# Kernel optimization log

Hardware: AMD Instinct MI355X
Metric: run time of the kernel (lower is better)

Reference implementation:

```python
import jax, jax.numpy as jnp
import numpy as np
import math

N_AGENTS = 512
TRAJ_LEN = 16
TAU = 2048          # obs_shape + n_actions = 1536 + 512
MSG = 32768         # messages_shape
HID = 512           # args.hidden_dim
DV = MSG // N_AGENTS  # 64, per-agent message dim


def setup_inputs() -> dict:
    key = jax.random.key(0)
    ks = jax.random.split(key, 8)
    s = 0.02
    return {
        "imagined_trajectory": jax.random.normal(ks[0], (TRAJ_LEN, N_AGENTS, TAU), jnp.float32),
        "received_messages": jax.random.normal(ks[1], (N_AGENTS, MSG), jnp.float32),
        "Wq": jax.random.normal(ks[2], (MSG, HID), jnp.float32) * s,
        "bq": jnp.zeros((HID,), jnp.float32),
        "Wk": jax.random.normal(ks[3], (TAU, HID), jnp.float32) * s,
        "bk": jnp.zeros((HID,), jnp.float32),
        "Wv": jax.random.normal(ks[4], (TAU, DV), jnp.float32) * s,
        "bv": jnp.zeros((DV,), jnp.float32),
    }


def reference(imagined_trajectory, received_messages, Wq, bq, Wk, bk, Wv, bv):
    # q: [N, H]
    q = received_messages @ Wq + bq
    T, N, tau = imagined_trajectory.shape
    taus = imagined_trajectory.reshape(T * N, tau)          # row j*N + i == (traj step j, agent i)
    k = (taus @ Wk + bk).reshape(T, N, HID)                 # [T, N, H]
    v = (taus @ Wv + bv).reshape(T, N, DV)                  # [T, N, Dv]
    # per-agent dot-product attention over trajectory steps (vectorized form of
    # the original double python loop: score[i, j] = dot(q[i], k[j*N+i]) / sqrt(H))
    scores = jnp.einsum("nh,tnh->nt", q, k) / math.sqrt(HID)  # [N, T]
    alpha = jax.nn.softmax(scores, axis=-1)
    messages = jnp.einsum("nt,tnd->nd", alpha, v)           # [N, Dv]
    return messages
```

## Files before the change

### kernel.cpp

```cpp
#include <hip/hip_runtime.h>
#include <hip/hip_fp16.h>

#define N_AG 512
#define TRAJ 16
#define TAU_ 2048
#define MSG_ 32768
#define HID_ 512
#define DV_ 64
#define NTOT 576
#define SPLITQ 32
#define LDS_K 40
#define BUFH (128 * LDS_K)

typedef _Float16 f16x8 __attribute__((ext_vector_type(8)));
typedef _Float16 f16x4 __attribute__((ext_vector_type(4)));
typedef _Float16 f16x2 __attribute__((ext_vector_type(2)));
typedef __fp16 h16x2 __attribute__((ext_vector_type(2)));
typedef float f32x4 __attribute__((ext_vector_type(4)));

#define VMCNT(n) asm volatile("s_waitcnt vmcnt(" #n ")" ::: "memory")
#define LGKM0    asm volatile("s_waitcnt lgkmcnt(0)" ::: "memory")
#define BAR()    __builtin_amdgcn_s_barrier()
#define SCHED0() __builtin_amdgcn_sched_barrier(0)

__device__ __forceinline__ void gload16(const void* g, void* l) {
    __builtin_amdgcn_global_load_lds(
        (const __attribute__((address_space(1))) void*)g,
        (__attribute__((address_space(3))) void*)l, 16, 0, 0);
}

__global__ __launch_bounds__(256) void prep(const float* __restrict__ Wk,
                                            const float* __restrict__ Wv,
                                            const float* __restrict__ bk,
                                            const float* __restrict__ bv,
                                            _Float16* __restrict__ Wt,
                                            float* __restrict__ bb)
{
    __shared__ float td[64][65];
    const int kt = blockIdx.x;
    const int nt = blockIdx.y;
    const int k0 = kt * 64;
    const bool isv = (nt == 8);
    const float* src = isv ? Wv : Wk;
    const int ldsrc = isv ? DV_ : HID_;
    const int ncol0 = isv ? 0 : nt * 64;
    for (int e = threadIdx.x; e < 4096; e += 256) {
        const int ki = e >> 6, ni = e & 63;
        td[ki][ni] = src[(size_t)(k0 + ki) * ldsrc + ncol0 + ni];
    }
    __syncthreads();
    for (int e = threadIdx.x; e < 4096; e += 256) {
        const int ni = e >> 6, ki = e & 63;
        Wt[(size_t)(nt * 64 + ni) * TAU_ + k0 + ki] = (_Float16)td[ki][ni];
    }
    if (kt == 0 && threadIdx.x < 64) {
        const int ng = nt * 64 + threadIdx.x;
        bb[ng] = isv ? bv[threadIdx.x] : bk[ng];
    }
}

__device__ __forceinline__ void gemm_tile128(
    _Float16* __restrict__ As, _Float16* __restrict__ Bs,
    const float* __restrict__ Ag, int lda,
    const float* __restrict__ Bg, int ldb,
    _Float16* __restrict__ Cg, int ldc, int K)
{
    const int tid = threadIdx.x;
    const int lane = tid & 63;
    const int wid = tid >> 6;
    const int wr = wid >> 1;
    const int wc = wid & 1;
    const int am = tid >> 1;
    const int ak = (tid & 1) << 4;
    const int btn = tid & 31;
    const int btk = tid >> 5;
    const int arow = wr * 64 + (lane & 15);
    const int brow = wc * 64 + (lane & 15);
    const int kblk = (lane >> 4) << 3;

    f32x4 acc[4][4];
#pragma unroll
    for (int mi = 0; mi < 4; ++mi)
#pragma unroll
        for (int ni = 0; ni < 4; ++ni)
            acc[mi][ni] = (f32x4){0.f, 0.f, 0.f, 0.f};

    float4 rA[8], rB[8];
    const int nt = K >> 5;

    auto load_stage = [&](float4 (&r)[8], int ks) {
        const float* ap = Ag + (size_t)am * lda + ks + ak;
#pragma unroll
        for (int i = 0; i < 4; ++i) r[i] = *(const float4*)(ap + 4 * i);
        const float* bp = Bg + (size_t)(ks + btk * 4) * ldb + btn * 4;
#pragma unroll
        for (int i = 0; i < 4; ++i) r[4 + i] = *(const float4*)(bp + (size_t)i * ldb);
    };
    auto write_stage = [&](float4 (&r)[8], int buf) {
        _Float16* abase = As + buf * BUFH + am * LDS_K + ak;
        const float* fa = (const float*)&r[0];
        f16x8 h0, h1;
#pragma unroll
        for (int i = 0; i < 8; ++i) { h0[i] = (_Float16)fa[i]; h1[i] = (_Float16)fa[8 + i]; }
        *(f16x8*)abase = h0;
        *(f16x8*)(abase + 8) = h1;
        const float* fb = (const float*)&r[4];
#pragma unroll
        for (int j = 0; j < 4; ++j) {
            f16x4 w;
#pragma unroll
            for (int i = 0; i < 4; ++i) w[i] = (_Float16)fb[i * 4 + j];
            *(f16x4*)(Bs + buf * BUFH + (btn * 4 + j) * LDS_K + btk * 4) = w;
        }
    };
    auto compute = [&](int buf) {
        const _Float16* ab = As + buf * BUFH;
        const _Float16* bbp = Bs + buf * BUFH;
        f16x8 af[4], bf[4];
#pragma unroll
        for (int mi = 0; mi < 4; ++mi)
            af[mi] = *(const f16x8*)(ab + (arow + mi * 16) * LDS_K + kblk);
#pragma unroll
        for (int ni = 0; ni < 4; ++ni)
            bf[ni] = *(const f16x8*)(bbp + (brow + ni * 16) * LDS_K + kblk);
#pragma unroll
        for (int mi = 0; mi < 4; ++mi)
#pragma unroll
            for (int ni = 0; ni < 4; ++ni)
                acc[mi][ni] = __builtin_amdgcn_mfma_f32_16x16x32_f16(
                    af[mi], bf[ni], acc[mi][ni], 0, 0, 0);
    };

    load_stage(rA, 0);
    load_stage(rB, 32);
    write_stage(rA, 0);
    __syncthreads();
    for (int t = 0; t < nt; t += 2) {
        if (t + 2 < nt) load_stage(rA, (t + 2) << 5);
        compute(0);
        if (t + 1 < nt) write_stage(rB, 1);
        __syncthreads();
        if (t + 3 < nt) load_stage(rB, (t + 3) << 5);
        compute(1);
        if (t + 2 < nt) write_stage(rA, 0);
        __syncthreads();
    }
#pragma unroll
    for (int mi = 0; mi < 4; ++mi)
#pragma unroll
        for (int ni = 0; ni < 4; ++ni) {
            const int row = wr * 64 + mi * 16 + ((lane >> 4) << 2);
            const int col = wc * 64 + ni * 16 + (lane & 15);
#pragma unroll
            for (int r = 0; r < 4; ++r)
                Cg[(size_t)(row + r) * ldc + col] = (_Float16)acc[mi][ni][r];
        }
}

__global__ __launch_bounds__(256, 2) void qgemm(const float* __restrict__ X,
                                                const float* __restrict__ Wq,
                                                _Float16* __restrict__ qpart)
{
    __shared__ __align__(16) _Float16 smem[4 * BUFH];
    const int b = blockIdx.x;
    const int w = (b & 7) * 64 + (b >> 3);
    const int s = w >> 4;
    const int bm = (w >> 2) & 3;
    const int bn = w & 3;
    const int KS = MSG_ / SPLITQ;
    gemm_tile128(smem, smem + 2 * BUFH,
                 X + (size_t)bm * 128 * MSG_ + s * KS, MSG_,
                 Wq + (size_t)(s * KS) * HID_ + bn * 128, HID_,
                 qpart + (size_t)s * (N_AG * HID_) + bm * 128 * HID_ + bn * 128, HID_,
                 KS);
}

__global__ __launch_bounds__(256, 2) void kvgemm(const float* __restrict__ A,
                                                 const _Float16* __restrict__ Wt,
                                                 const float* __restrict__ bb,
                                                 _Float16* __restrict__ cmat)
{
    __shared__ __align__(1024) char smem[32768];
    const int tid = threadIdx.x;
    const int l = tid & 63;
    const int w = tid >> 6;

    const int b = blockIdx.x;
    const int wsw = (b & 7) * 48 + (b >> 3);
    const int bm = wsw / 3;
    const int bn = wsw % 3;
    const int m0 = bm * 64;
    const int n0 = bn * 192;

    const int arow = tid >> 2;
    const int aslot = (tid & 3) ^ ((tid >> 3) & 3);
    const float* ag = A + (size_t)(m0 + arow) * TAU_ + (tid & 3) * 8;
    char* const alds = smem + arow * 64 + aslot * 16;

    const int bsrcc = (l & 3) ^ ((l >> 3) & 3);

    const int r15 = l & 15;
    const int swz = ((l >> 4) ^ ((r15 >> 1) & 3)) * 16;

    f32x4 acc[4][3];
#pragma unroll
    for (int mi = 0; mi < 4; ++mi)
#pragma unroll
        for (int ni = 0; ni < 3; ++ni)
            acc[mi][ni] = (f32x4){0.f, 0.f, 0.f, 0.f};

    float4 r0[2], r1[2];

    auto aload = [&](float4 (&r)[2], int t) {
        const float* p = ag + t * 32;
        r[0] = *(const float4*)(p);
        r[1] = *(const float4*)(p + 4);
    };
    auto awrite = [&](float4 (&r)[2], int parity) {
        union { h16x2 h2[4]; f16x8 v; } u;
        const float* f = (const float*)&r[0];
        u.h2[0] = __builtin_amdgcn_cvt_pkrtz(f[0], f[1]);
        u.h2[1] = __builtin_amdgcn_cvt_pkrtz(f[2], f[3]);
        u.h2[2] = __builtin_amdgcn_cvt_pkrtz(f[4], f[5]);
        u.h2[3] = __builtin_amdgcn_cvt_pkrtz(f[6], f[7]);
        *(f16x8*)(alds + parity * 4096) = u.v;
    };
    auto bdma = [&](int t, int parity) {
        char* base = smem + 8192 + parity * 12288;
#pragma unroll
        for (int jj = 0; jj < 3; ++jj) {
            const int j = w * 3 + jj;
            const int row = 16 * j + (l >> 2);
            const _Float16* gp = Wt + (size_t)(n0 + row) * TAU_ + t * 32 + bsrcc * 8;
            gload16(gp, base + j * 1024);
        }
    };
    auto compute = [&](int parity) {
        const char* ab = smem + parity * 4096;
        const char* bbp = smem + 8192 + parity * 12288;
        f16x8 af[4], bf[3];
#pragma unroll
        for (int mi = 0; mi < 4; ++mi)
            af[mi] = *(const f16x8*)(ab + (mi * 16 + r15) * 64 + swz);
#pragma unroll
        for (int ni = 0; ni < 3; ++ni)
            bf[ni] = *(const f16x8*)(bbp + (w * 48 + ni * 16 + r15) * 64 + swz);
        __builtin_amdgcn_s_setprio(1);
#pragma unroll
        for (int mi = 0; mi < 4; ++mi)
#pragma unroll
            for (int ni = 0; ni < 3; ++ni)
                acc[mi][ni] = __builtin_amdgcn_mfma_f32_16x16x32_f16(
                    af[mi], bf[ni], acc[mi][ni], 0, 0, 0);
        __builtin_amdgcn_s_setprio(0);
    };

    bdma(0, 0); aload(r0, 0);
    bdma(1, 1); aload(r1, 1);
    VMCNT(5);
    awrite(r0, 0);
    LGKM0;

    for (int t = 0; t < 62; t += 2) {
        BAR(); SCHED0();
        compute(0);
        SCHED0(); BAR();
        bdma(t + 2, 0); aload(r0, t + 2);
        VMCNT(5);
        awrite(r1, 1);
        LGKM0;

        BAR(); SCHED0();
        compute(1);
        SCHED0(); BAR();
        bdma(t + 3, 1); aload(r1, t + 3);
        VMCNT(5);
        awrite(r0, 0);
        LGKM0;
    }
    BAR(); SCHED0();
    compute(0);
    SCHED0(); BAR();
    VMCNT(0);
    awrite(r1, 1);
    LGKM0;
    BAR(); SCHED0();
    compute(1);

#pragma unroll
    for (int mi = 0; mi < 4; ++mi)
#pragma unroll
        for (int ni = 0; ni < 3; ++ni) {
            const int row = m0 + mi * 16 + ((l >> 4) << 2);
            const int col = n0 + w * 48 + ni * 16 + r15;
            const float badd = bb[col];
#pragma unroll
            for (int r = 0; r < 4; ++r)
                cmat[(size_t)(row + r) * NTOT + col] = (_Float16)(acc[mi][ni][r] + badd);
        }
}

__global__ __launch_bounds__(256) void attn(const _Float16* __restrict__ qpart,
                                            const _Float16* __restrict__ cmat,
                                            const float* __restrict__ bq,
                                            const float* __restrict__ bv,
                                            float* __restrict__ out)
{
    const int n = blockIdx.x;
    const int tid = threadIdx.x;
    __shared__ float qs[HID_];
    __shared__ float scr[TRAJ];

    {
        const int h2 = tid * 2;
        float a0 = bq[h2], a1 = bq[h2 + 1];
#pragma unroll
        for (int s = 0; s < SPLITQ; ++s) {
            f16x2 p = *(const f16x2*)(qpart + (size_t)s * (N_AG * HID_) + n * HID_ + h2);
            a0 += (float)p[0];
            a1 += (float)p[1];
        }
        qs[h2] = a0;
        qs[h2 + 1] = a1;
    }
    __syncthreads();

    const int w = tid >> 6;
    const int lane = tid & 63;
#pragma unroll
    for (int tt = 0; tt < 4; ++tt) {
        const int t = w * 4 + tt;
        const _Float16* kr = cmat + (size_t)(t * N_AG + n) * NTOT;
        const int h0 = lane * 8;
        f16x8 kv = *(const f16x8*)(kr + h0);
        float p = 0.f;
#pragma unroll
        for (int i = 0; i < 8; ++i) p += qs[h0 + i] * (float)kv[i];
#pragma unroll
        for (int off = 32; off > 0; off >>= 1) p += __shfl_xor(p, off);
        if (lane == 0) scr[t] = p;
    }
    __syncthreads();

    const float inv = 0.04419417382415922f;
    float sv[TRAJ];
    float mx = -1e30f;
#pragma unroll
    for (int t = 0; t < TRAJ; ++t) { sv[t] = scr[t] * inv; mx = fmaxf(mx, sv[t]); }
    float ssum = 0.f;
#pragma unroll
    for (int t = 0; t < TRAJ; ++t) { sv[t] = expf(sv[t] - mx); ssum += sv[t]; }
    const float rs = 1.f / ssum;

    if (tid < DV_) {
        float o = bv[tid];
#pragma unroll
        for (int t = 0; t < TRAJ; ++t)
            o += sv[t] * rs * (float)cmat[(size_t)(t * N_AG + n) * NTOT + HID_ + tid];
        out[n * DV_ + tid] = o;
    }
}

extern "C" void kernel_launch(void* const* d_in, const int* in_sizes, int n_in,
                              void* d_out, int out_size, void* d_ws, size_t ws_size,
                              hipStream_t stream)
{
    const float* traj = (const float*)d_in[0];
    const float* msgs = (const float*)d_in[1];
    const float* Wq   = (const float*)d_in[2];
    const float* bq   = (const float*)d_in[3];
    const float* Wk   = (const float*)d_in[4];
    const float* bk   = (const float*)d_in[5];
    const float* Wv   = (const float*)d_in[6];
    const float* bv   = (const float*)d_in[7];
    float* out = (float*)d_out;

    _Float16* qpart = (_Float16*)d_ws;
    _Float16* cmat  = qpart + (size_t)SPLITQ * N_AG * HID_;
    _Float16* Wt    = cmat + (size_t)TRAJ * N_AG * NTOT;
    float*    bb    = (float*)(Wt + (size_t)NTOT * TAU_);

    prep<<<dim3(32, 9), 256, 0, stream>>>(Wk, Wv, bk, bv, Wt, bb);
    qgemm<<<512, 256, 0, stream>>>(msgs, Wq, qpart);
    kvgemm<<<384, 256, 0, stream>>>(traj, Wt, bb, cmat);
    attn<<<512, 256, 0, stream>>>(qpart, cmat, bq, bv, out);
}
```

Before: 95.78 us.

## Deepen kvgemm pipeline from double to quad-buffered LDS stages

Changes the kv projection GEMM from a 2-stage to a 4-stage software pipeline. Three tiles of the fp32 A operand are held in registers and the B tiles are DMA'd into LDS ahead of compute, so more global-memory latency is hidden. LDS use doubles to 64KB per block, which may limit blocks per CU under the launch bounds of 2 and adds register pressure from the extra float4 staging sets.

```diff
diff --git a/kernel.cpp b/kernel.cpp
--- a/kernel.cpp
+++ b/kernel.cpp
@@ -180,7 +180,7 @@
                                                  const float* __restrict__ bb,
                                                  _Float16* __restrict__ cmat)
 {
-    __shared__ __align__(1024) char smem[32768];
+    __shared__ __align__(1024) char smem[65536];
     const int tid = threadIdx.x;
     const int l = tid & 63;
     const int w = tid >> 6;
@@ -209,24 +209,24 @@
         for (int ni = 0; ni < 3; ++ni)
             acc[mi][ni] = (f32x4){0.f, 0.f, 0.f, 0.f};
 
-    float4 r0[2], r1[2];
+    float4 r0[2], r1[2], r2[2], r3[2];
 
     auto aload = [&](float4 (&r)[2], int t) {
         const float* p = ag + t * 32;
         r[0] = *(const float4*)(p);
         r[1] = *(const float4*)(p + 4);
     };
-    auto awrite = [&](float4 (&r)[2], int parity) {
+    auto awrite = [&](float4 (&r)[2], int set) {
         union { h16x2 h2[4]; f16x8 v; } u;
         const float* f = (const float*)&r[0];
         u.h2[0] = __builtin_amdgcn_cvt_pkrtz(f[0], f[1]);
         u.h2[1] = __builtin_amdgcn_cvt_pkrtz(f[2], f[3]);
         u.h2[2] = __builtin_amdgcn_cvt_pkrtz(f[4], f[5]);
         u.h2[3] = __builtin_amdgcn_cvt_pkrtz(f[6], f[7]);
-        *(f16x8*)(alds + parity * 4096) = u.v;
-    };
-    auto bdma = [&](int t, int parity) {
-        char* base = smem + 8192 + parity * 12288;
+        *(f16x8*)(alds + set * 4096) = u.v;
+    };
+    auto bdma = [&](int t, int set) {
+        char* base = smem + 16384 + set * 12288;
 #pragma unroll
         for (int jj = 0; jj < 3; ++jj) {
             const int j = w * 3 + jj;
@@ -235,9 +235,9 @@
             gload16(gp, base + j * 1024);
         }
     };
-    auto compute = [&](int parity) {
-        const char* ab = smem + parity * 4096;
-        const char* bbp = smem + 8192 + parity * 12288;
+    auto compute = [&](int set) {
+        const char* ab = smem + set * 4096;
+        const char* bbp = smem + 16384 + set * 12288;
         f16x8 af[4], bf[3];
 #pragma unroll
         for (int mi = 0; mi < 4; ++mi)
@@ -257,35 +257,47 @@
 
     bdma(0, 0); aload(r0, 0);
     bdma(1, 1); aload(r1, 1);
-    VMCNT(5);
+    bdma(2, 2); aload(r2, 2);
+    VMCNT(10);
     awrite(r0, 0);
     LGKM0;
 
-    for (int t = 0; t < 62; t += 2) {
-        BAR(); SCHED0();
-        compute(0);
-        SCHED0(); BAR();
-        bdma(t + 2, 0); aload(r0, t + 2);
-        VMCNT(5);
-        awrite(r1, 1);
-        LGKM0;
-
-        BAR(); SCHED0();
-        compute(1);
-        SCHED0(); BAR();
-        bdma(t + 3, 1); aload(r1, t + 3);
-        VMCNT(5);
-        awrite(r0, 0);
-        LGKM0;
-    }
-    BAR(); SCHED0();
+#define MPHASE(p, pn1, pn3, tt)                         \
+    bdma((tt) + 3, pn3); aload(r##pn3, (tt) + 3);       \
+    VMCNT(10);                                          \
+    awrite(r##pn1, pn1);                                \
+    LGKM0; BAR(); SCHED0();                             \
+    compute(p);                                         \
+    SCHED0(); BAR();
+
+    for (int g = 0; g < 15; ++g) {
+        const int t = g * 4;
+        MPHASE(0, 1, 3, t + 0)
+        MPHASE(1, 2, 0, t + 1)
+        MPHASE(2, 3, 1, t + 2)
+        MPHASE(3, 0, 2, t + 3)
+    }
+#undef MPHASE
+    bdma(63, 3); aload(r3, 63);
+    VMCNT(10);
+    awrite(r1, 1);
+    LGKM0; BAR(); SCHED0();
     compute(0);
     SCHED0(); BAR();
+
+    VMCNT(5);
+    awrite(r2, 2);
+    LGKM0; BAR(); SCHED0();
+    compute(1);
+    SCHED0(); BAR();
+
     VMCNT(0);
-    awrite(r1, 1);
-    LGKM0;
-    BAR(); SCHED0();
-    compute(1);
+    awrite(r3, 3);
+    LGKM0; BAR(); SCHED0();
+    compute(2);
+    SCHED0(); BAR();
+
+    compute(3);
 
 #pragma unroll
     for (int mi = 0; mi < 4; ++mi)
```

After: 95.82 us. Within noise of the previous version (+0.0%).
